# Optimization experiments

Measured on AMD Instinct MI355X. Metric: run time of the kernel, lower is better.

The kernel has to match this reference:

```python
import jax, jax.numpy as jnp
import numpy as np
import math

B, S, D, H = 4, 2048, 1024, 16
HD = D // H  # head_dim = 64


def _rope_tables(max_len, half_dim, theta=10000.0):
    inv_freq = 1.0 / (theta ** (jnp.arange(0, half_dim, dtype=jnp.float32) / half_dim))
    ang = jnp.arange(max_len, dtype=jnp.float32)[:, None] * inv_freq[None, :]  # [max_len, half_dim]
    return jnp.cos(ang), jnp.sin(ang)


def _apply_rope(x, cos, sin):
    # x: [B, H, S, HD]; cos/sin: [S, HD/2]
    x1, x2 = x[..., ::2], x[..., 1::2]
    # matches torch.cat([x1*cos - x2*sin, x1*sin + x2*cos], dim=-1)
    return jnp.concatenate([x1 * cos - x2 * sin, x1 * sin + x2 * cos], axis=-1)


def setup_inputs() -> dict:
    key = jax.random.key(0)
    kx, kq, ko = jax.random.split(key, 3)
    x = jax.random.normal(kx, (B, S, D), dtype=jnp.float32)
    Wqkv = jax.random.normal(kq, (D, 3 * D), dtype=jnp.float32) / math.sqrt(D)
    Wout = jax.random.normal(ko, (D, D), dtype=jnp.float32) / math.sqrt(D)
    cos, sin = _rope_tables(S, HD // 2)
    # causal additive mask, per-batch as in module signature [B, S, S]
    causal = jnp.where(jnp.tril(jnp.ones((S, S), dtype=bool)), 0.0, -1e9).astype(jnp.float32)
    mask = jnp.broadcast_to(causal, (B, S, S))
    return {"x": x, "cos": cos, "sin": sin, "mask": mask, "Wqkv": Wqkv, "Wout": Wout}


def reference(x, cos, sin, mask, Wqkv, Wout):
    b, s, d = x.shape
    qkv = x @ Wqkv  # [B, S, 3D]
    q, k, v = jnp.split(qkv, 3, axis=-1)
    def to_heads(t):
        return t.reshape(b, s, H, HD).transpose(0, 2, 1, 3)  # [B, H, S, HD]
    q, k, v = to_heads(q), to_heads(k), to_heads(v)
    q = _apply_rope(q, cos[:s], sin[:s])
    k = _apply_rope(k, cos[:s], sin[:s])
    scores = jnp.einsum("bhqd,bhkd->bhqk", q, k) / math.sqrt(HD)
    attn = jax.nn.softmax(scores + mask[:, None, :, :], axis=-1)
    out = jnp.einsum("bhqk,bhkd->bhqd", attn, v)  # [B, H, S, HD]
    out = out.transpose(0, 2, 1, 3).reshape(b, s, d)
    return out @ Wout
```

## Files before the change

### kernel.cpp

```cpp
#include <hip/hip_runtime.h>
#include <hip/hip_bf16.h>
#include <stdint.h>

#define B_   4
#define S_   2048
#define D_   1024
#define H_   16
#define HD_  64
#define BH_  (B_*H_)
#define MROWS (B_*S_)

typedef short  short8  __attribute__((ext_vector_type(8)));
typedef float  floatx4 __attribute__((ext_vector_type(4)));

__device__ __forceinline__ ushort f2bf(float f) {
    union { float f; uint32_t u; } v; v.f = f;
    uint32_t u = v.u;
    return (ushort)((u + 0x7FFFu + ((u >> 16) & 1u)) >> 16);
}
__device__ __forceinline__ float u2f(uint32_t u) {
    union { uint32_t u; float f; } v; v.u = u; return v.f;
}
__device__ __forceinline__ uint32_t f2u(float f) {
    union { float f; uint32_t u; } v; v.f = f; return v.u;
}

__device__ __forceinline__ void gl_lds16(const ushort* g, ushort* l) {
    __builtin_amdgcn_global_load_lds(
        (const __attribute__((address_space(1))) unsigned int*)g,
        (__attribute__((address_space(3))) unsigned int*)l,
        16, 0, 0);
}

__global__ __launch_bounds__(256)
void k_prep(const float* __restrict__ x, const float* __restrict__ Wqkv,
            const float* __restrict__ Wout,
            ushort* __restrict__ Xbf, ushort* __restrict__ WqkvT, ushort* __restrict__ WoutT) {
    __shared__ float tile[32][33];
    int blk = blockIdx.x;
    int tid = threadIdx.x;
    if (blk >= 4096) {
        int i = (blk - 4096) * 1024 + tid * 4;
        float4 f = *(const float4*)(x + i);
        ushort4 o; o.x = f2bf(f.x); o.y = f2bf(f.y); o.z = f2bf(f.z); o.w = f2bf(f.w);
        *(ushort4*)(Xbf + i) = o;
        return;
    }
    const float* in; ushort* out; int R, C, bx, by;
    if (blk < 3072) { in = Wqkv; out = WqkvT; R = D_; C = 3 * D_; bx = (blk % 96) * 32; by = (blk / 96) * 32; }
    else            { int b2 = blk - 3072; in = Wout; out = WoutT; R = D_; C = D_; bx = (b2 % 32) * 32; by = (b2 / 32) * 32; }
    int tx = tid & 31, ty = tid >> 5;
    #pragma unroll
    for (int j = 0; j < 32; j += 8)
        tile[ty + j][tx] = in[(size_t)(by + ty + j) * C + bx + tx];
    __syncthreads();
    #pragma unroll
    for (int j = 0; j < 32; j += 8)
        out[(size_t)(bx + ty + j) * R + by + tx] = f2bf(tile[tx][ty + j]);
}

#define BM 128
#define BN 128
#define BK 64

template<int EPI>
__global__ __launch_bounds__(256)
void k_gemm(const ushort* __restrict__ A, const ushort* __restrict__ Bt,
            float* __restrict__ outF,
            ushort* __restrict__ q_out, ushort* __restrict__ k_out, ushort* __restrict__ v_out,
            int M, int N, int K) {
    __shared__ __align__(16) ushort As[BM * 64];
    __shared__ __align__(16) ushort Bs[BN * 64];
    int tid  = threadIdx.x;
    int lane = tid & 63;
    int wave = tid >> 6;
    int quad = lane >> 4;
    int l16  = lane & 15;
    int bm = blockIdx.y * BM;
    int bn = blockIdx.x * BN;
    int wm = (wave >> 1) * 64;
    int wn = (wave & 1) * 64;

    floatx4 acc[4][4] = {};

    for (int k0 = 0; k0 < K; k0 += BK) {
        __syncthreads();
        #pragma unroll
        for (int i = 0; i < 4; i++) {
            int c   = i * 256 + tid;
            int row = c >> 3;
            int gc  = (c & 7) ^ (row & 7);
            gl_lds16(&A[(size_t)(bm + row) * K + k0 + gc * 8],  &As[c * 8]);
            gl_lds16(&Bt[(size_t)(bn + row) * K + k0 + gc * 8], &Bs[c * 8]);
        }
        __syncthreads();
        #pragma unroll
        for (int kk = 0; kk < 2; kk++) {
            short8 af[4], bf[4];
            #pragma unroll
            for (int mt = 0; mt < 4; mt++)
                af[mt] = *(const short8*)&As[(wm + mt * 16 + l16) * 64 +
                                             (((kk * 4 + quad) ^ (l16 & 7)) << 3)];
            #pragma unroll
            for (int nt = 0; nt < 4; nt++)
                bf[nt] = *(const short8*)&Bs[(wn + nt * 16 + l16) * 64 +
                                             (((kk * 4 + quad) ^ (l16 & 7)) << 3)];
            #pragma unroll
            for (int mt = 0; mt < 4; mt++)
                #pragma unroll
                for (int nt = 0; nt < 4; nt++)
                    acc[mt][nt] = __builtin_amdgcn_mfma_f32_16x16x32_bf16(af[mt], bf[nt], acc[mt][nt], 0, 0, 0);
        }
    }

    #pragma unroll
    for (int mt = 0; mt < 4; mt++)
        #pragma unroll
        for (int nt = 0; nt < 4; nt++)
            #pragma unroll
            for (int r = 0; r < 4; r++) {
                int row = bm + wm + mt * 16 + quad * 4 + r;
                int col = bn + wn + nt * 16 + l16;
                float v = acc[mt][nt][r];
                if (EPI == 0) {
                    int which = col >> 10;
                    int rem   = col & 1023;
                    int h  = rem >> 6, hd = rem & 63;
                    int b  = row >> 11, s  = row & 2047;
                    size_t idx = ((size_t)(b * H_ + h) * S_ + s) * HD_ + hd;
                    ushort bv = f2bf(v);
                    ushort* dst = (which == 0) ? q_out : (which == 1) ? k_out : v_out;
                    dst[idx] = bv;
                } else {
                    outF[(size_t)row * N + col] = v;
                }
            }
}

__global__ __launch_bounds__(256)
void k_ropevt(ushort* __restrict__ Q, ushort* __restrict__ Kv,
              const ushort* __restrict__ Vb, ushort* __restrict__ VbT,
              const float* __restrict__ cosT, const float* __restrict__ sinT) {
    __shared__ __align__(16) ushort t[64 * 72];
    int blk = blockIdx.x;
    int tid = threadIdx.x;
    if (blk < 32768) {
        int wid  = (blk * 256 + tid) >> 6;
        int lane = tid & 63;
        int s  = wid & (S_ - 1);
        int bh = wid >> 11;
        int i  = lane & 31;
        float c  = cosT[s * 32 + i];
        float sn = sinT[s * 32 + i];
        size_t base = ((size_t)bh * S_ + s) * HD_;

        uint32_t uq = *(const uint32_t*)&Q[base + 2 * i];
        float x1 = u2f(uq << 16), x2 = u2f(uq & 0xFFFF0000u);
        float o  = (lane < 32) ? (x1 * c - x2 * sn) : (x1 * sn + x2 * c);
        Q[base + lane] = f2bf(o * 0.1803368801f);

        uint32_t uk = *(const uint32_t*)&Kv[base + 2 * i];
        x1 = u2f(uk << 16); x2 = u2f(uk & 0xFFFF0000u);
        o  = (lane < 32) ? (x1 * c - x2 * sn) : (x1 * sn + x2 * c);
        Kv[base + lane] = f2bf(o);
        return;
    }
    int b2 = blk - 32768;
    int bh = b2 >> 5;
    int s0 = (b2 & 31) * 64;
    int ss = tid >> 2, c0 = (tid & 3) * 16;
    size_t base = (size_t)bh * S_ * HD_;
    *(uint4*)&t[ss * 72 + c0]     = *(const uint4*)&Vb[base + (size_t)(s0 + ss) * HD_ + c0];
    *(uint4*)&t[ss * 72 + c0 + 8] = *(const uint4*)&Vb[base + (size_t)(s0 + ss) * HD_ + c0 + 8];
    __syncthreads();
    int hd = tid >> 2, q0 = (tid & 3) * 16;
    ushort tmp[16];
    #pragma unroll
    for (int e = 0; e < 16; e++) tmp[e] = t[(q0 + e) * 72 + hd];
    size_t obase = (size_t)bh * HD_ * S_ + (size_t)hd * S_ + s0 + q0;
    *(uint4*)&VbT[obase]     = *(const uint4*)&tmp[0];
    *(uint4*)&VbT[obase + 8] = *(const uint4*)&tmp[8];
}

__global__ __launch_bounds__(256, 4)
void k_attn(const ushort* __restrict__ Q, const ushort* __restrict__ K,
            const ushort* __restrict__ VT, ushort* __restrict__ O) {
    __shared__ __align__(16) ushort Ks[64 * 64];
    __shared__ __align__(16) ushort Vt[64 * 64];
    __shared__ __align__(16) ushort Pst[4][32 * 64];

    const int PI[16] = {15,14,11,10, 12,13,8,9, 2,3,6,7, 1,0,5,4};

    int tid  = threadIdx.x;
    int lane = tid & 63;
    int wave = tid >> 6;
    int quad = lane >> 4;
    int l16  = lane & 15;

    int bh   = blockIdx.x & 63;
    int qblk = PI[blockIdx.x >> 6];
    int qb0  = qblk * 128;
    size_t hbase = (size_t)bh * S_ * HD_;
    size_t vbase = (size_t)bh * HD_ * S_;

    int mrow[2] = { qb0 + wave * 16, qb0 + 64 + wave * 16 };

    short8 qf[2][2];
    #pragma unroll
    for (int m = 0; m < 2; m++)
        #pragma unroll
        for (int h = 0; h < 2; h++)
            qf[m][h] = *(const short8*)&Q[hbase + (size_t)(mrow[m] + l16) * HD_ + quad * 8 + h * 32];

    short8 ones;
    #pragma unroll
    for (int e = 0; e < 8; e++) ones[e] = (short)0x3F80;

    floatx4 acc[2][4] = {};
    floatx4 accl[2] = {};

    int c0r = tid >> 3;
    int c1r = (256 + tid) >> 3;
    const ushort* kp0 = &K[hbase + (size_t)c0r * HD_ + (((tid & 7) ^ (c0r & 7)) << 3)];
    const ushort* kp1 = &K[hbase + (size_t)c1r * HD_ + (((tid & 7) ^ (c1r & 7)) << 3)];
    const ushort* vp0 = &VT[vbase + (size_t)c0r * S_ + (((tid & 7) ^ (c0r & 7)) << 3)];
    const ushort* vp1 = &VT[vbase + (size_t)c1r * S_ + (((tid & 7) ^ (c1r & 7)) << 3)];

    int nk = 2 * qblk + 2;
    for (int kb = 0; kb < nk; kb++) {
        int k0 = kb * 64;
        __syncthreads();
        gl_lds16(kp0, &Ks[tid * 8]);
        gl_lds16(kp1, &Ks[(256 + tid) * 8]);
        gl_lds16(vp0, &Vt[tid * 8]);
        gl_lds16(vp1, &Vt[(256 + tid) * 8]);
        kp0 += 64 * HD_; kp1 += 64 * HD_; vp0 += 64; vp1 += 64;
        __syncthreads();

        bool act[2] = { k0 <= mrow[0] + 15, k0 <= mrow[1] + 15 };

        #pragma unroll
        for (int m = 0; m < 2; m++) {
            if (!act[m]) continue;
            floatx4 sc[4] = {};
            #pragma unroll
            for (int kt = 0; kt < 4; kt++)
                #pragma unroll
                for (int h = 0; h < 2; h++) {
                    short8 kf = *(const short8*)&Ks[(kt * 16 + l16) * 64 +
                                                    (((h * 4 + quad) ^ (l16 & 7)) << 3)];
                    sc[kt] = __builtin_amdgcn_mfma_f32_16x16x32_bf16(kf, qf[m][h], sc[kt], 0, 0, 0);
                }
            bool needMask = (k0 + 63 > mrow[m]);
            int qr = mrow[m] + l16;
            #pragma unroll
            for (int kt = 0; kt < 4; kt++) {
                float p[4];
                #pragma unroll
                for (int r = 0; r < 4; r++) {
                    float v = exp2f(sc[kt][r]);
                    if (needMask) {
                        int kc = k0 + kt * 16 + quad * 4 + r;
                        if (kc > qr) v = 0.0f;
                    }
                    p[r] = v;
                }
                uint2 pk;
                pk.x = __builtin_amdgcn_perm(f2u(p[1]) + 0x8000u, f2u(p[0]) + 0x8000u, 0x07060302u);
                pk.y = __builtin_amdgcn_perm(f2u(p[3]) + 0x8000u, f2u(p[2]) + 0x8000u, 0x07060302u);
                int pc = (kt * 4 + quad) ^ (l16 & 14);
                *(uint2*)&Pst[wave][(m * 16 + l16) * 64 + pc * 4] = pk;
            }
        }

        #pragma unroll
        for (int k2 = 0; k2 < 2; k2++) {
            short8 vb[4];
            #pragma unroll
            for (int nt = 0; nt < 4; nt++)
                vb[nt] = *(const short8*)&Vt[(nt * 16 + l16) * 64 +
                                             (((k2 * 4 + quad) ^ (l16 & 7)) << 3)];
            #pragma unroll
            for (int m = 0; m < 2; m++) {
                if (!act[m]) continue;
                int pe = (k2 * 8 + quad * 2) ^ (l16 & 14);
                short8 pa = *(const short8*)&Pst[wave][(m * 16 + l16) * 64 + pe * 4];
                #pragma unroll
                for (int nt = 0; nt < 4; nt++)
                    acc[m][nt] = __builtin_amdgcn_mfma_f32_16x16x32_bf16(pa, vb[nt], acc[m][nt], 0, 0, 0);
                accl[m] = __builtin_amdgcn_mfma_f32_16x16x32_bf16(pa, ones, accl[m], 0, 0, 0);
            }
        }
    }

    int b = bh >> 4, h = bh & 15;
    #pragma unroll
    for (int m = 0; m < 2; m++)
        #pragma unroll
        for (int r = 0; r < 4; r++) {
            float inv = 1.0f / accl[m][r];
            int qr = mrow[m] + quad * 4 + r;
            #pragma unroll
            for (int nt = 0; nt < 4; nt++)
                O[((size_t)(b * S_ + qr)) * D_ + h * HD_ + nt * 16 + l16] = f2bf(acc[m][nt][r] * inv);
        }
}

extern "C" void kernel_launch(void* const* d_in, const int* in_sizes, int n_in,
                              void* d_out, int out_size, void* d_ws, size_t ws_size,
                              hipStream_t stream) {
    const float* x    = (const float*)d_in[0];
    const float* cosT = (const float*)d_in[1];
    const float* sinT = (const float*)d_in[2];
    const float* Wqkv = (const float*)d_in[4];
    const float* Wout = (const float*)d_in[5];
    float* out = (float*)d_out;

    ushort* ws = (ushort*)d_ws;
    ushort* Xbf    = ws;
    ushort* WqkvT  = Xbf    + (size_t)MROWS * D_;
    ushort* WoutT  = WqkvT  + (size_t)3 * D_ * D_;
    ushort* Qb     = WoutT  + (size_t)D_ * D_;
    ushort* Kb     = Qb     + (size_t)BH_ * S_ * HD_;
    ushort* Vb     = Kb     + (size_t)BH_ * S_ * HD_;
    ushort* VbT    = Vb     + (size_t)BH_ * S_ * HD_;
    ushort* AO     = Xbf;

    k_prep<<<12288, 256, 0, stream>>>(x, Wqkv, Wout, Xbf, WqkvT, WoutT);
    k_gemm<0><<<dim3(3 * D_ / BN, MROWS / BM), 256, 0, stream>>>(Xbf, WqkvT, nullptr, Qb, Kb, Vb,
                                                                 MROWS, 3 * D_, D_);
    k_ropevt<<<34816, 256, 0, stream>>>(Qb, Kb, Vb, VbT, cosT, sinT);
    k_attn<<<1024, 256, 0, stream>>>(Qb, Kb, VbT, AO);
    k_gemm<1><<<dim3(D_ / BN, MROWS / BM), 256, 0, stream>>>(AO, WoutT, out, nullptr, nullptr, nullptr,
                                                             MROWS, D_, D_);
}
```

Baseline: 307.3 us.

## Double-buffer K/V tiles in LDS and process P·V per query sub-tile

Adds a second LDS buffer for K and V so the async global-to-LDS loads for the next key block are issued before computing on the current block. This removes the second barrier and overlaps load latency with MFMA work. The P staging buffer is halved by doing the P·V product right after each 16-row sub-tile's softmax, at the cost of re-reading V fragments from LDS for each sub-tile. The query-block launch order also changes from a custom permutation to a plain descending order. Total LDS use rises, which can limit occupancy.

```diff
diff --git a/kernel.cpp b/kernel.cpp
--- a/kernel.cpp
+++ b/kernel.cpp
@@ -185,11 +185,9 @@
 __global__ __launch_bounds__(256, 4)
 void k_attn(const ushort* __restrict__ Q, const ushort* __restrict__ K,
             const ushort* __restrict__ VT, ushort* __restrict__ O) {
-    __shared__ __align__(16) ushort Ks[64 * 64];
-    __shared__ __align__(16) ushort Vt[64 * 64];
-    __shared__ __align__(16) ushort Pst[4][32 * 64];
-
-    const int PI[16] = {15,14,11,10, 12,13,8,9, 2,3,6,7, 1,0,5,4};
+    __shared__ __align__(16) ushort Ks[2][64 * 64];
+    __shared__ __align__(16) ushort Vt[2][64 * 64];
+    __shared__ __align__(16) ushort Pst[4][16 * 64];
 
     int tid  = threadIdx.x;
     int lane = tid & 63;
@@ -198,7 +196,7 @@
     int l16  = lane & 15;
 
     int bh   = blockIdx.x & 63;
-    int qblk = PI[blockIdx.x >> 6];
+    int qblk = 15 - (blockIdx.x >> 6);
     int qb0  = qblk * 128;
     size_t hbase = (size_t)bh * S_ * HD_;
     size_t vbase = (size_t)bh * HD_ * S_;
@@ -227,15 +225,25 @@
     const ushort* vp1 = &VT[vbase + (size_t)c1r * S_ + (((tid & 7) ^ (c1r & 7)) << 3)];
 
     int nk = 2 * qblk + 2;
+
+    gl_lds16(kp0, &Ks[0][tid * 8]);
+    gl_lds16(kp1, &Ks[0][(256 + tid) * 8]);
+    gl_lds16(vp0, &Vt[0][tid * 8]);
+    gl_lds16(vp1, &Vt[0][(256 + tid) * 8]);
+    kp0 += 64 * HD_; kp1 += 64 * HD_; vp0 += 64; vp1 += 64;
+
     for (int kb = 0; kb < nk; kb++) {
         int k0 = kb * 64;
         __syncthreads();
-        gl_lds16(kp0, &Ks[tid * 8]);
-        gl_lds16(kp1, &Ks[(256 + tid) * 8]);
-        gl_lds16(vp0, &Vt[tid * 8]);
-        gl_lds16(vp1, &Vt[(256 + tid) * 8]);
-        kp0 += 64 * HD_; kp1 += 64 * HD_; vp0 += 64; vp1 += 64;
-        __syncthreads();
+        if (kb + 1 < nk) {
+            int nb = (kb + 1) & 1;
+            gl_lds16(kp0, &Ks[nb][tid * 8]);
+            gl_lds16(kp1, &Ks[nb][(256 + tid) * 8]);
+            gl_lds16(vp0, &Vt[nb][tid * 8]);
+            gl_lds16(vp1, &Vt[nb][(256 + tid) * 8]);
+            kp0 += 64 * HD_; kp1 += 64 * HD_; vp0 += 64; vp1 += 64;
+        }
+        int cur = kb & 1;
 
         bool act[2] = { k0 <= mrow[0] + 15, k0 <= mrow[1] + 15 };
 
@@ -247,8 +255,8 @@
             for (int kt = 0; kt < 4; kt++)
                 #pragma unroll
                 for (int h = 0; h < 2; h++) {
-                    short8 kf = *(const short8*)&Ks[(kt * 16 + l16) * 64 +
-                                                    (((h * 4 + quad) ^ (l16 & 7)) << 3)];
+                    short8 kf = *(const short8*)&Ks[cur][(kt * 16 + l16) * 64 +
+                                                        (((h * 4 + quad) ^ (l16 & 7)) << 3)];
                     sc[kt] = __builtin_amdgcn_mfma_f32_16x16x32_bf16(kf, qf[m][h], sc[kt], 0, 0, 0);
                 }
             bool needMask = (k0 + 63 > mrow[m]);
@@ -269,25 +277,18 @@
                 pk.x = __builtin_amdgcn_perm(f2u(p[1]) + 0x8000u, f2u(p[0]) + 0x8000u, 0x07060302u);
                 pk.y = __builtin_amdgcn_perm(f2u(p[3]) + 0x8000u, f2u(p[2]) + 0x8000u, 0x07060302u);
                 int pc = (kt * 4 + quad) ^ (l16 & 14);
-                *(uint2*)&Pst[wave][(m * 16 + l16) * 64 + pc * 4] = pk;
+                *(uint2*)&Pst[wave][l16 * 64 + pc * 4] = pk;
             }
-        }
-
-        #pragma unroll
-        for (int k2 = 0; k2 < 2; k2++) {
-            short8 vb[4];
-            #pragma unroll
-            for (int nt = 0; nt < 4; nt++)
-                vb[nt] = *(const short8*)&Vt[(nt * 16 + l16) * 64 +
-                                             (((k2 * 4 + quad) ^ (l16 & 7)) << 3)];
-            #pragma unroll
-            for (int m = 0; m < 2; m++) {
-                if (!act[m]) continue;
+            #pragma unroll
+            for (int k2 = 0; k2 < 2; k2++) {
                 int pe = (k2 * 8 + quad * 2) ^ (l16 & 14);
-                short8 pa = *(const short8*)&Pst[wave][(m * 16 + l16) * 64 + pe * 4];
+                short8 pa = *(const short8*)&Pst[wave][l16 * 64 + pe * 4];
                 #pragma unroll
-                for (int nt = 0; nt < 4; nt++)
-                    acc[m][nt] = __builtin_amdgcn_mfma_f32_16x16x32_bf16(pa, vb[nt], acc[m][nt], 0, 0, 0);
+                for (int nt = 0; nt < 4; nt++) {
+                    short8 vb = *(const short8*)&Vt[cur][(nt * 16 + l16) * 64 +
+                                                         (((k2 * 4 + quad) ^ (l16 & 7)) << 3)];
+                    acc[m][nt] = __builtin_amdgcn_mfma_f32_16x16x32_bf16(pa, vb, acc[m][nt], 0, 0, 0);
+                }
                 accl[m] = __builtin_amdgcn_mfma_f32_16x16x32_bf16(pa, ones, accl[m], 0, 0, 0);
             }
         }
```

New measurement: 319.6 us. +4.0%, slower.
